# Kernel tuning notes

Hardware: AMD Instinct MI355X
Metric: run time of the kernel (lower is better)

## Reference

```python
import jax, jax.numpy as jnp
import numpy as np

D, H, S, T, NN, IN_CH, FEAT, SPA, OUT, NL, FF, E = 512, 8, 64, 32, 512, 32, 64, 32, 32, 4, 2048, 16384
NEG = 0.2  # leaky relu negative slope (GATv2 default and alpha)

def _ln(x, g, b):
    m = x.mean(-1, keepdims=True)
    v = ((x - m) ** 2).mean(-1, keepdims=True)
    return (x - m) / jnp.sqrt(v + 1e-5) * g + b

def _posenc(L):
    pos = jnp.arange(L, dtype=jnp.float32)[:, None]
    div = jnp.exp(-jnp.log(10000.0) * jnp.arange(0, D, 2, dtype=jnp.float32) / D)
    pe = jnp.zeros((L, D), jnp.float32)
    pe = pe.at[:, 0::2].set(jnp.sin(pos * div)).at[:, 1::2].set(jnp.cos(pos * div))
    return pe[:, None, :]  # (L,1,D), seq-first

def _mha(xq, xkv, wqkv, bqkv, wo, bo, mask=None):
    Lq, N, _ = xq.shape
    Lk = xkv.shape[0]
    dh = D // H
    wq, wk, wv = jnp.split(wqkv, 3, axis=1)
    bq, bk, bv = jnp.split(bqkv, 3)
    q = (xq @ wq + bq).reshape(Lq, N, H, dh)
    k = (xkv @ wk + bk).reshape(Lk, N, H, dh)
    v = (xkv @ wv + bv).reshape(Lk, N, H, dh)
    s = jnp.einsum('qnhd,knhd->nhqk', q, k) / jnp.sqrt(jnp.float32(dh))
    if mask is not None:
        s = s + mask
    a = jax.nn.softmax(s, -1)
    o = jnp.einsum('nhqk,knhd->qnhd', a, v).reshape(Lq, N, D)
    return o @ wo + bo

def _gatv2(x, wl, wr, bl, br, att, bias, e_src, e_dst):
    # GATv2: e_ij = a . leakyrelu(Wl x_j + Wr x_i); softmax over incoming edges of i; out_i = sum alpha_ij Wl x_j
    n = x.shape[0]
    h, c = att.shape
    xl = (x @ wl + bl).reshape(n, h, c)
    xr = (x @ wr + br).reshape(n, h, c)
    z = jax.nn.leaky_relu(xl[e_src] + xr[e_dst], NEG)   # (E,H,C)
    e = jnp.einsum('ehc,hc->eh', z, att)                # (E,H)
    m = jax.lax.stop_gradient(jax.ops.segment_max(e, e_dst, num_segments=n))
    ex = jnp.exp(e - m[e_dst])
    den = jax.ops.segment_sum(ex, e_dst, num_segments=n)
    alpha = ex / den[e_dst]
    out = jax.ops.segment_sum(alpha[..., None] * xl[e_src], e_dst, num_segments=n)
    return out.reshape(n, h * c) + bias

def _fwd(src, tgt, w_enc_in, b_enc_in, w_dec_in, b_dec_in, w_map, b_map,
         enc_qkv_w, enc_qkv_b, enc_out_w, enc_out_b, enc_ff1_w, enc_ff1_b, enc_ff2_w, enc_ff2_b,
         enc_ln1_g, enc_ln1_b, enc_ln2_g, enc_ln2_b, enc_fn_g, enc_fn_b,
         dec_sa_qkv_w, dec_sa_qkv_b, dec_sa_out_w, dec_sa_out_b,
         dec_ca_qkv_w, dec_ca_qkv_b, dec_ca_out_w, dec_ca_out_b,
         dec_ff1_w, dec_ff1_b, dec_ff2_w, dec_ff2_b,
         dec_ln1_g, dec_ln1_b, dec_ln2_g, dec_ln2_b, dec_ln3_g, dec_ln3_b, dec_fn_g, dec_fn_b,
         g1_wl, g1_wr, g1_bl, g1_br, g1_att, g1_bias,
         g2_wl, g2_wr, g2_bl, g2_br, g2_att, g2_bias,
         edge_index):
    # temporal transformer (eval mode, dropout off), seq-first (L, N, D)
    x = src @ w_enc_in + b_enc_in + _posenc(S)
    for i in range(NL):  # post-norm encoder, relu FFN (nn.TransformerEncoderLayer defaults)
        a = _mha(x, x, enc_qkv_w[i], enc_qkv_b[i], enc_out_w[i], enc_out_b[i])
        x = _ln(x + a, enc_ln1_g[i], enc_ln1_b[i])
        f = jax.nn.relu(x @ enc_ff1_w[i] + enc_ff1_b[i]) @ enc_ff2_w[i] + enc_ff2_b[i]
        x = _ln(x + f, enc_ln2_g[i], enc_ln2_b[i])
    mem = _ln(x, enc_fn_g, enc_fn_b)
    causal = jnp.triu(jnp.full((T, T), -1e9, jnp.float32), k=1)
    y = tgt @ w_dec_in + b_dec_in + _posenc(T)
    for i in range(NL):
        a = _mha(y, y, dec_sa_qkv_w[i], dec_sa_qkv_b[i], dec_sa_out_w[i], dec_sa_out_b[i], causal)
        y = _ln(y + a, dec_ln1_g[i], dec_ln1_b[i])
        a = _mha(y, mem, dec_ca_qkv_w[i], dec_ca_qkv_b[i], dec_ca_out_w[i], dec_ca_out_b[i])
        y = _ln(y + a, dec_ln2_g[i], dec_ln2_b[i])
        f = jax.nn.relu(y @ dec_ff1_w[i] + dec_ff1_b[i]) @ dec_ff2_w[i] + dec_ff2_b[i]
        y = _ln(y + f, dec_ln3_g[i], dec_ln3_b[i])
    y = _ln(y, dec_fn_g, dec_fn_b) @ w_map + b_map  # (T, N, FEAT)
    e_src, e_dst = edge_index[0], edge_index[1]
    def spatial(xt):  # two-layer GATv2 per time step, then elu (concat=True branch)
        h1 = _gatv2(xt, g1_wl, g1_wr, g1_bl, g1_br, g1_att, g1_bias, e_src, e_dst)
        h2 = _gatv2(h1, g2_wl, g2_wr, g2_bl, g2_br, g2_att, g2_bias, e_src, e_dst)
        return jax.nn.elu(h2)
    g = jax.vmap(spatial)(y)  # (T, N, H*OUT)
    return jax.nn.relu(g)


def setup_inputs():
    ks = iter(jax.random.split(jax.random.key(0), 100))
    def w(shape, s=0.05):
        return jax.random.normal(next(ks), shape, jnp.float32) * s
    inp = {}
    inp['src'] = jax.random.normal(next(ks), (S, NN, IN_CH), jnp.float32)
    inp['tgt'] = jax.random.normal(next(ks), (T, NN, FEAT), jnp.float32)
    inp['w_enc_in'] = w((IN_CH, D)); inp['b_enc_in'] = jnp.zeros((D,))
    inp['w_dec_in'] = w((FEAT, D)); inp['b_dec_in'] = jnp.zeros((D,))
    inp['w_map'] = w((D, FEAT)); inp['b_map'] = jnp.zeros((FEAT,))
    inp['enc_qkv_w'] = w((NL, D, 3 * D)); inp['enc_qkv_b'] = jnp.zeros((NL, 3 * D))
    inp['enc_out_w'] = w((NL, D, D)); inp['enc_out_b'] = jnp.zeros((NL, D))
    inp['enc_ff1_w'] = w((NL, D, FF)); inp['enc_ff1_b'] = jnp.zeros((NL, FF))
    inp['enc_ff2_w'] = w((NL, FF, D)); inp['enc_ff2_b'] = jnp.zeros((NL, D))
    inp['enc_ln1_g'] = jnp.ones((NL, D)); inp['enc_ln1_b'] = jnp.zeros((NL, D))
    inp['enc_ln2_g'] = jnp.ones((NL, D)); inp['enc_ln2_b'] = jnp.zeros((NL, D))
    inp['enc_fn_g'] = jnp.ones((D,)); inp['enc_fn_b'] = jnp.zeros((D,))
    inp['dec_sa_qkv_w'] = w((NL, D, 3 * D)); inp['dec_sa_qkv_b'] = jnp.zeros((NL, 3 * D))
    inp['dec_sa_out_w'] = w((NL, D, D)); inp['dec_sa_out_b'] = jnp.zeros((NL, D))
    inp['dec_ca_qkv_w'] = w((NL, D, 3 * D)); inp['dec_ca_qkv_b'] = jnp.zeros((NL, 3 * D))
    inp['dec_ca_out_w'] = w((NL, D, D)); inp['dec_ca_out_b'] = jnp.zeros((NL, D))
    inp['dec_ff1_w'] = w((NL, D, FF)); inp['dec_ff1_b'] = jnp.zeros((NL, FF))
    inp['dec_ff2_w'] = w((NL, FF, D)); inp['dec_ff2_b'] = jnp.zeros((NL, D))
    inp['dec_ln1_g'] = jnp.ones((NL, D)); inp['dec_ln1_b'] = jnp.zeros((NL, D))
    inp['dec_ln2_g'] = jnp.ones((NL, D)); inp['dec_ln2_b'] = jnp.zeros((NL, D))
    inp['dec_ln3_g'] = jnp.ones((NL, D)); inp['dec_ln3_b'] = jnp.zeros((NL, D))
    inp['dec_fn_g'] = jnp.ones((D,)); inp['dec_fn_b'] = jnp.zeros((D,))
    inp['g1_wl'] = w((FEAT, H * SPA)); inp['g1_wr'] = w((FEAT, H * SPA))
    inp['g1_bl'] = jnp.zeros((H * SPA,)); inp['g1_br'] = jnp.zeros((H * SPA,))
    inp['g1_att'] = w((H, SPA), 0.1); inp['g1_bias'] = jnp.zeros((H * SPA,))
    inp['g2_wl'] = w((H * SPA, H * OUT)); inp['g2_wr'] = w((H * SPA, H * OUT))
    inp['g2_bl'] = jnp.zeros((H * OUT,)); inp['g2_br'] = jnp.zeros((H * OUT,))
    inp['g2_att'] = w((H, OUT), 0.1); inp['g2_bias'] = jnp.zeros((H * OUT,))
    inp['edge_index'] = jax.random.randint(next(ks), (2, E), 0, NN)
    return inp


def reference(src, tgt, w_enc_in, b_enc_in, w_dec_in, b_dec_in, w_map, b_map,
              enc_qkv_w, enc_qkv_b, enc_out_w, enc_out_b, enc_ff1_w, enc_ff1_b, enc_ff2_w, enc_ff2_b,
              enc_ln1_g, enc_ln1_b, enc_ln2_g, enc_ln2_b, enc_fn_g, enc_fn_b,
              dec_sa_qkv_w, dec_sa_qkv_b, dec_sa_out_w, dec_sa_out_b,
              dec_ca_qkv_w, dec_ca_qkv_b, dec_ca_out_w, dec_ca_out_b,
              dec_ff1_w, dec_ff1_b, dec_ff2_w, dec_ff2_b,
              dec_ln1_g, dec_ln1_b, dec_ln2_g, dec_ln2_b, dec_ln3_g, dec_ln3_b, dec_fn_g, dec_fn_b,
              g1_wl, g1_wr, g1_bl, g1_br, g1_att, g1_bias,
              g2_wl, g2_wr, g2_bl, g2_br, g2_att, g2_bias,
              edge_index):
    return _fwd(src, tgt, w_enc_in, b_enc_in, w_dec_in, b_dec_in, w_map, b_map,
                enc_qkv_w, enc_qkv_b, enc_out_w, enc_out_b, enc_ff1_w, enc_ff1_b, enc_ff2_w, enc_ff2_b,
                enc_ln1_g, enc_ln1_b, enc_ln2_g, enc_ln2_b, enc_fn_g, enc_fn_b,
                dec_sa_qkv_w, dec_sa_qkv_b, dec_sa_out_w, dec_sa_out_b,
                dec_ca_qkv_w, dec_ca_qkv_b, dec_ca_out_w, dec_ca_out_b,
                dec_ff1_w, dec_ff1_b, dec_ff2_w, dec_ff2_b,
                dec_ln1_g, dec_ln1_b, dec_ln2_g, dec_ln2_b, dec_ln3_g, dec_ln3_b, dec_fn_g, dec_fn_b,
                g1_wl, g1_wr, g1_bl, g1_br, g1_att, g1_bias,
                g2_wl, g2_wr, g2_bl, g2_br, g2_att, g2_bias,
                edge_index)
```

## Files before the change

kernel.cpp:

```cpp
#include <hip/hip_runtime.h>
#include <hip/hip_bf16.h>

#define NHEAD 8
#define SLEN 64
#define TLEN 32
#define NNODE 512
#define NEDGE 16384
#define NLAYER 4

typedef __attribute__((ext_vector_type(8))) __bf16 bf16x8;
typedef __attribute__((ext_vector_type(4))) __bf16 bf16x4;
typedef __attribute__((ext_vector_type(4))) float  f32x4;

__device__ __forceinline__ void gload16(const void* g, void* l)
{
    __builtin_amdgcn_global_load_lds(
        (const __attribute__((address_space(1))) void*)g,
        (__attribute__((address_space(3))) void*)l, 16, 0, 0);
}

template<int BN>
__global__ __launch_bounds__(256) void gemm_bf16(
    const __bf16* __restrict__ A, int lda,
    const __bf16* __restrict__ Bt, int ldb,
    const float* __restrict__ bias,
    const __bf16* __restrict__ Res,
    float* __restrict__ Cf, __bf16* __restrict__ Cb, int ldc,
    int M, int N, int K, int outMode)
{
    constexpr int FM = (BN == 128) ? 4 : 2;
    __shared__ __bf16 As[128 * 64];
    __shared__ __bf16 Bs[BN * 64];
    const int tid  = threadIdx.x;
    const int wid  = tid >> 6;
    const int lane = tid & 63;
    const int wr = (BN == 128) ? (wid >> 1) : wid;
    const int wc = (BN == 128) ? (wid & 1) : 0;
    const int m0 = blockIdx.y * 128, n0 = blockIdx.x * BN;

    const int srow = wid * 8 + (lane >> 3);
    const int scol = (lane & 7) * 8;
    const int lr = lane & 15;
    const int kg = (lane >> 4) * 8;

    f32x4 acc[FM][4];
    #pragma unroll
    for (int m = 0; m < FM; ++m)
        #pragma unroll
        for (int n = 0; n < 4; ++n)
            acc[m][n] = (f32x4){0.0f, 0.0f, 0.0f, 0.0f};

    for (int k0 = 0; k0 < K; k0 += 64) {
        #pragma unroll
        for (int g = 0; g < 4; ++g) {
            const __bf16* ga = A + (size_t)(m0 + g * 32 + srow) * lda + k0 + scol;
            gload16(ga, &As[(g * 32 + wid * 8) * 64]);
        }
        #pragma unroll
        for (int g = 0; g < BN / 32; ++g) {
            const __bf16* gb = Bt + (size_t)(n0 + g * 32 + srow) * ldb + k0 + scol;
            gload16(gb, &Bs[(g * 32 + wid * 8) * 64]);
        }
        __syncthreads();
        #pragma unroll
        for (int kk = 0; kk < 64; kk += 32) {
            bf16x8 fa[FM], fb[4];
            #pragma unroll
            for (int m = 0; m < FM; ++m)
                fa[m] = *reinterpret_cast<const bf16x8*>(
                    &As[(wr * (16 * FM) + m * 16 + lr) * 64 + kk + kg]);
            #pragma unroll
            for (int n = 0; n < 4; ++n)
                fb[n] = *reinterpret_cast<const bf16x8*>(
                    &Bs[(wc * 64 + n * 16 + lr) * 64 + kk + kg]);
            #pragma unroll
            for (int m = 0; m < FM; ++m)
                #pragma unroll
                for (int n = 0; n < 4; ++n)
                    acc[m][n] = __builtin_amdgcn_mfma_f32_16x16x32_bf16(
                        fa[m], fb[n], acc[m][n], 0, 0, 0);
        }
        __syncthreads();
    }

    const int cr = (lane >> 4) * 4;
    const int cc = lane & 15;
    #pragma unroll
    for (int n = 0; n < 4; ++n) {
        const int gcol = n0 + wc * 64 + n * 16 + cc;
        const float bb = bias[gcol];
        #pragma unroll
        for (int m = 0; m < FM; ++m) {
            #pragma unroll
            for (int j = 0; j < 4; ++j) {
                const int grow = m0 + wr * (16 * FM) + m * 16 + cr + j;
                float v = acc[m][n][j] + bb;
                if (Res) v += (float)Res[(size_t)grow * ldc + gcol];
                if (outMode == 1 || outMode == 2) v = fmaxf(v, 0.0f);
                if (outMode >= 2) Cb[(size_t)grow * ldc + gcol] = (__bf16)v;
                else              Cf[(size_t)grow * ldc + gcol] = v;
            }
        }
    }
}

__global__ __launch_bounds__(256) void gemm_bias(
    const float* __restrict__ A, int lda,
    const float* __restrict__ B, int ldb,
    const float* __restrict__ bias,
    float* __restrict__ C, int ldc,
    int M, int N, int K, int relu)
{
    __shared__ float As[16][68];
    __shared__ float Bs[16][68];
    const int tid = threadIdx.x;
    const int tx = tid & 15, ty = tid >> 4;
    const int m0 = blockIdx.y * 64, n0 = blockIdx.x * 64;
    const int liA_m = tid >> 2;
    const int liA_k = (tid & 3) * 4;
    const int liB_n = (tid & 15) * 4;
    const int liB_k = tid >> 4;
    float acc[4][4] = {};
    for (int k0 = 0; k0 < K; k0 += 16) {
        float4 av = *reinterpret_cast<const float4*>(&A[(size_t)(m0 + liA_m) * lda + k0 + liA_k]);
        float4 bv = *reinterpret_cast<const float4*>(&B[(size_t)(k0 + liB_k) * ldb + n0 + liB_n]);
        As[liA_k + 0][liA_m] = av.x;
        As[liA_k + 1][liA_m] = av.y;
        As[liA_k + 2][liA_m] = av.z;
        As[liA_k + 3][liA_m] = av.w;
        *reinterpret_cast<float4*>(&Bs[liB_k][liB_n]) = bv;
        __syncthreads();
        #pragma unroll
        for (int kk = 0; kk < 16; ++kk) {
            float4 a4 = *reinterpret_cast<const float4*>(&As[kk][ty * 4]);
            float4 b4 = *reinterpret_cast<const float4*>(&Bs[kk][tx * 4]);
            float a[4] = {a4.x, a4.y, a4.z, a4.w};
            float b[4] = {b4.x, b4.y, b4.z, b4.w};
            #pragma unroll
            for (int i = 0; i < 4; ++i)
                #pragma unroll
                for (int j = 0; j < 4; ++j)
                    acc[i][j] += a[i] * b[j];
        }
        __syncthreads();
    }
    #pragma unroll
    for (int i = 0; i < 4; ++i) {
        const int m = m0 + ty * 4 + i;
        #pragma unroll
        for (int j = 0; j < 4; ++j) {
            const int n = n0 + tx * 4 + j;
            float v = acc[i][j] + bias[n];
            if (relu) v = fmaxf(v, 0.0f);
            C[(size_t)m * ldc + n] = v;
        }
    }
}

__global__ __launch_bounds__(256) void transpose_w(
    const float* __restrict__ in, __bf16* __restrict__ out, int K, int N)
{
    __shared__ __bf16 t[32][33];
    const int l = blockIdx.z;
    in  += (size_t)l * K * N;
    out += (size_t)l * K * N;
    const int k0 = blockIdx.y * 32, n0 = blockIdx.x * 32;
    const int tx = threadIdx.x & 31, ty = threadIdx.x >> 5;
    #pragma unroll
    for (int i = 0; i < 32; i += 8)
        t[ty + i][tx] = (__bf16)in[(size_t)(k0 + ty + i) * N + n0 + tx];
    __syncthreads();
    #pragma unroll
    for (int i = 0; i < 32; i += 8)
        out[(size_t)(n0 + ty + i) * K + k0 + tx] = t[tx][ty + i];
}

__global__ __launch_bounds__(256) void conv_bf16(
    const float* __restrict__ in, __bf16* __restrict__ out, int total4)
{
    const int i = blockIdx.x * 256 + threadIdx.x;
    if (i >= total4) return;
    const float4 v = *reinterpret_cast<const float4*>(&in[(size_t)i * 4]);
    bf16x4 w;
    w[0] = (__bf16)v.x; w[1] = (__bf16)v.y; w[2] = (__bf16)v.z; w[3] = (__bf16)v.w;
    *reinterpret_cast<bf16x4*>(&out[(size_t)i * 4]) = w;
}

__global__ __launch_bounds__(256) void permute_in(
    const float* __restrict__ in, float* __restrict__ out, int L, int CH, int total)
{
    const int idx = blockIdx.x * 256 + threadIdx.x;
    if (idx >= total) return;
    const int c = idx % CH;
    const int r = idx / CH;
    const int n = r & 511;
    const int l = r >> 9;
    out[((size_t)n * L + l) * CH + c] = in[idx];
}

__global__ __launch_bounds__(256) void permute_F(
    const __bf16* __restrict__ in, __bf16* __restrict__ out)
{
    const int idx = blockIdx.x * 256 + threadIdx.x;
    if (idx >= 16384 * 64) return;
    const int c = idx & 63;
    const int r = idx >> 6;
    const int n = r >> 5;
    const int t = r & 31;
    out[((size_t)(t * 512 + n)) * 64 + c] = in[idx];
}

template<int LQ, int LK, bool CAUSAL>
__global__ __launch_bounds__(64) void attn_mfma(
    const __bf16* __restrict__ Q, int ldq,
    const __bf16* __restrict__ Kp, int ldk,
    const __bf16* __restrict__ Vp, int ldv,
    __bf16* __restrict__ O, int ldo)
{
    constexpr int QF = LQ / 16, KF = LK / 16;
    constexpr int PSTR = LK + 8;
    __shared__ __bf16 Vt[64 * PSTR];
    __shared__ __bf16 Ps[LQ * PSTR];
    const int n = blockIdx.x >> 3;
    const int h = blockIdx.x & 7;
    const int lane = threadIdx.x;
    const int lr = lane & 15;
    const int g4 = lane >> 4;
    const int kg = g4 * 8;

    if (lane < LK) {
        #pragma unroll
        for (int j = 0; j < 8; ++j) {
            bf16x8 vv = *reinterpret_cast<const bf16x8*>(
                &Vp[(size_t)(n * LK + lane) * ldv + h * 64 + j * 8]);
            #pragma unroll
            for (int e = 0; e < 8; ++e)
                Vt[(j * 8 + e) * PSTR + lane] = vv[e];
        }
    }

    f32x4 s[QF][KF];
    #pragma unroll
    for (int qi = 0; qi < QF; ++qi)
        #pragma unroll
        for (int ki = 0; ki < KF; ++ki)
            s[qi][ki] = (f32x4){0.0f, 0.0f, 0.0f, 0.0f};
    #pragma unroll
    for (int kk = 0; kk < 64; kk += 32) {
        bf16x8 fa[QF], fb[KF];
        #pragma unroll
        for (int qi = 0; qi < QF; ++qi)
            fa[qi] = *reinterpret_cast<const bf16x8*>(
                &Q[(size_t)(n * LQ + qi * 16 + lr) * ldq + h * 64 + kk + kg]);
        #pragma unroll
        for (int ki = 0; ki < KF; ++ki)
            fb[ki] = *reinterpret_cast<const bf16x8*>(
                &Kp[(size_t)(n * LK + ki * 16 + lr) * ldk + h * 64 + kk + kg]);
        #pragma unroll
        for (int qi = 0; qi < QF; ++qi)
            #pragma unroll
            for (int ki = 0; ki < KF; ++ki)
                s[qi][ki] = __builtin_amdgcn_mfma_f32_16x16x32_bf16(fa[qi], fb[ki], s[qi][ki], 0, 0, 0);
    }

    float inv_s[QF][4];
    #pragma unroll
    for (int qi = 0; qi < QF; ++qi) {
        #pragma unroll
        for (int j = 0; j < 4; ++j) {
            const int row = qi * 16 + g4 * 4 + j;
            float mx = -1e30f;
            #pragma unroll
            for (int ki = 0; ki < KF; ++ki) {
                float v = s[qi][ki][j] * 0.125f;
                if (CAUSAL) { const int col = ki * 16 + lr; if (col > row) v = -1e30f; }
                s[qi][ki][j] = v;
                mx = fmaxf(mx, v);
            }
            #pragma unroll
            for (int d = 1; d < 16; d <<= 1) mx = fmaxf(mx, __shfl_xor(mx, d));
            float sum = 0.0f;
            #pragma unroll
            for (int ki = 0; ki < KF; ++ki) {
                const float p = __expf(s[qi][ki][j] - mx);
                s[qi][ki][j] = p;
                sum += p;
            }
            #pragma unroll
            for (int d = 1; d < 16; d <<= 1) sum += __shfl_xor(sum, d);
            inv_s[qi][j] = 1.0f / sum;
            #pragma unroll
            for (int ki = 0; ki < KF; ++ki)
                Ps[row * PSTR + ki * 16 + lr] = (__bf16)s[qi][ki][j];
        }
    }
    __syncthreads();

    f32x4 o[QF][4];
    #pragma unroll
    for (int qi = 0; qi < QF; ++qi)
        #pragma unroll
        for (int di = 0; di < 4; ++di)
            o[qi][di] = (f32x4){0.0f, 0.0f, 0.0f, 0.0f};
    #pragma unroll
    for (int kk = 0; kk < LK; kk += 32) {
        bf16x8 fa[QF], fb[4];
        #pragma unroll
        for (int qi = 0; qi < QF; ++qi)
            fa[qi] = *reinterpret_cast<const bf16x8*>(&Ps[(qi * 16 + lr) * PSTR + kk + kg]);
        #pragma unroll
        for (int di = 0; di < 4; ++di)
            fb[di] = *reinterpret_cast<const bf16x8*>(&Vt[(di * 16 + lr) * PSTR + kk + kg]);
        #pragma unroll
        for (int qi = 0; qi < QF; ++qi)
            #pragma unroll
            for (int di = 0; di < 4; ++di)
                o[qi][di] = __builtin_amdgcn_mfma_f32_16x16x32_bf16(fa[qi], fb[di], o[qi][di], 0, 0, 0);
    }
    #pragma unroll
    for (int qi = 0; qi < QF; ++qi)
        #pragma unroll
        for (int di = 0; di < 4; ++di)
            #pragma unroll
            for (int j = 0; j < 4; ++j) {
                const int row = qi * 16 + g4 * 4 + j;
                O[(size_t)(n * LQ + row) * ldo + h * 64 + di * 16 + lr] =
                    (__bf16)(o[qi][di][j] * inv_s[qi][j]);
            }
}

template<bool HASR, bool F32OUT>
__global__ __launch_bounds__(256) void ln_bf16(
    const __bf16* __restrict__ X, const __bf16* __restrict__ Rb,
    const float* __restrict__ g, const float* __restrict__ b,
    __bf16* __restrict__ outb, float* __restrict__ outf, int ntok)
{
    const int wid = threadIdx.x >> 6, lane = threadIdx.x & 63;
    const int row = blockIdx.x * 4 + wid;
    if (row >= ntok) return;
    const size_t base = (size_t)row * 512;
    const int c0 = lane * 8;
    const bf16x8 xv = *reinterpret_cast<const bf16x8*>(&X[base + c0]);
    float v[8];
    float s = 0.0f;
    if (HASR) {
        const bf16x8 rv = *reinterpret_cast<const bf16x8*>(&Rb[base + c0]);
        #pragma unroll
        for (int j = 0; j < 8; ++j) { v[j] = (float)xv[j] + (float)rv[j]; s += v[j]; }
    } else {
        #pragma unroll
        for (int j = 0; j < 8; ++j) { v[j] = (float)xv[j]; s += v[j]; }
    }
    #pragma unroll
    for (int d = 32; d >= 1; d >>= 1) s += __shfl_xor(s, d, 64);
    const float mean = s * (1.0f / 512.0f);
    float vs = 0.0f;
    #pragma unroll
    for (int j = 0; j < 8; ++j) { const float d = v[j] - mean; vs += d * d; }
    #pragma unroll
    for (int d = 32; d >= 1; d >>= 1) vs += __shfl_xor(vs, d, 64);
    const float rstd = rsqrtf(vs * (1.0f / 512.0f) + 1e-5f);
    const float4 g0 = *reinterpret_cast<const float4*>(&g[c0]);
    const float4 g1 = *reinterpret_cast<const float4*>(&g[c0 + 4]);
    const float4 b0 = *reinterpret_cast<const float4*>(&b[c0]);
    const float4 b1 = *reinterpret_cast<const float4*>(&b[c0 + 4]);
    const float gg[8] = {g0.x, g0.y, g0.z, g0.w, g1.x, g1.y, g1.z, g1.w};
    const float bb[8] = {b0.x, b0.y, b0.z, b0.w, b1.x, b1.y, b1.z, b1.w};
    if (F32OUT) {
        f32x4 o0, o1;
        #pragma unroll
        for (int j = 0; j < 4; ++j) o0[j] = (v[j] - mean) * rstd * gg[j] + bb[j];
        #pragma unroll
        for (int j = 0; j < 4; ++j) o1[j] = (v[4 + j] - mean) * rstd * gg[4 + j] + bb[4 + j];
        *reinterpret_cast<f32x4*>(&outf[base + c0]) = o0;
        *reinterpret_cast<f32x4*>(&outf[base + c0 + 4]) = o1;
    } else {
        bf16x8 w;
        #pragma unroll
        for (int j = 0; j < 8; ++j) w[j] = (__bf16)((v[j] - mean) * rstd * gg[j] + bb[j]);
        *reinterpret_cast<bf16x8*>(&outb[base + c0]) = w;
    }
}

__global__ __launch_bounds__(256) void add_posenc(float* __restrict__ x, int L, int total)
{
    const int idx = blockIdx.x * 256 + threadIdx.x;
    if (idx >= total) return;
    const int d = idx & 511;
    const int row = idx >> 9;
    const int l = row % L;
    const int i2 = d & ~1;
    const float freq = expf(-9.210340371976184f * (float)i2 / 512.0f);
    const float a = (float)l * freq;
    x[idx] += (d & 1) ? cosf(a) : sinf(a);
}

__global__ void zero_ints(int* __restrict__ p, int n)
{
    const int i = blockIdx.x * 256 + threadIdx.x;
    if (i < n) p[i] = 0;
}

__global__ void count_deg(const int* __restrict__ edst, int* __restrict__ deg)
{
    const int e = blockIdx.x * 256 + threadIdx.x;
    if (e < NEDGE) atomicAdd(&deg[edst[e]], 1);
}

__global__ void scan512(const int* __restrict__ deg, int* __restrict__ off)
{
    __shared__ int s[512];
    const int tid = threadIdx.x;
    s[tid] = deg[tid];
    __syncthreads();
    for (int d = 1; d < 512; d <<= 1) {
        const int t = (tid >= d) ? s[tid - d] : 0;
        __syncthreads();
        s[tid] += t;
        __syncthreads();
    }
    off[tid + 1] = s[tid];
    if (tid == 0) off[0] = 0;
}

__global__ void fill_eid(const int* __restrict__ edst, const int* __restrict__ off,
                         int* __restrict__ cur, int* __restrict__ eid)
{
    const int e = blockIdx.x * 256 + threadIdx.x;
    if (e < NEDGE) {
        const int d = edst[e];
        const int pos = off[d] + atomicAdd(&cur[d], 1);
        eid[pos] = e;
    }
}

template<bool FINAL>
__global__ __launch_bounds__(256) void gatv2_kernel(
    const float* __restrict__ xl, const float* __restrict__ xr,
    const float* __restrict__ att, const float* __restrict__ bias,
    const int* __restrict__ off, const int* __restrict__ eid,
    const int* __restrict__ esrc,
    __bf16* __restrict__ outb16, float* __restrict__ outd)
{
    const int blk = blockIdx.x;
    const int i = blk & (NNODE - 1);
    const int t = blk >> 9;
    const int tid = threadIdx.x;
    const float xrv = xr[(size_t)blk * 256 + tid];
    const float av = att[tid];
    const int e0 = off[i], e1 = off[i + 1];
    float m = -1e30f, den = 0.0f, acc = 0.0f;
    for (int idx = e0; idx < e1; ++idx) {
        const int e = eid[idx];
        const int s = esrc[e];
        const float xlv = xl[((size_t)(t * 512 + s)) * 256 + tid];
        float z = xlv + xrv;
        z = (z > 0.0f) ? z : 0.2f * z;
        float w = z * av;
        #pragma unroll
        for (int d = 16; d >= 1; d >>= 1) w += __shfl_xor(w, d, 32);
        const float mn = fmaxf(m, w);
        const float sc = __expf(m - mn);
        const float p  = __expf(w - mn);
        den = den * sc + p;
        acc = acc * sc + p * xlv;
        m = mn;
    }
    float o = (den > 0.0f) ? acc / den : 0.0f;
    o += bias[tid];
    if (FINAL) {
        o = fmaxf(o, 0.0f);
        outd[(size_t)blk * 256 + tid] = o;
    } else {
        outb16[(size_t)blk * 256 + tid] = (__bf16)o;
    }
}

extern "C" void kernel_launch(void* const* d_in, const int* in_sizes, int n_in,
                              void* d_out, int out_size, void* d_ws, size_t ws_size,
                              hipStream_t stream)
{
    const float* src       = (const float*)d_in[0];
    const float* tgt       = (const float*)d_in[1];
    const float* w_enc_in  = (const float*)d_in[2];
    const float* b_enc_in  = (const float*)d_in[3];
    const float* w_dec_in  = (const float*)d_in[4];
    const float* b_dec_in  = (const float*)d_in[5];
    const float* w_map     = (const float*)d_in[6];
    const float* b_map     = (const float*)d_in[7];
    const float* enc_qkv_w = (const float*)d_in[8];
    const float* enc_qkv_b = (const float*)d_in[9];
    const float* enc_out_w = (const float*)d_in[10];
    const float* enc_out_b = (const float*)d_in[11];
    const float* enc_ff1_w = (const float*)d_in[12];
    const float* enc_ff1_b = (const float*)d_in[13];
    const float* enc_ff2_w = (const float*)d_in[14];
    const float* enc_ff2_b = (const float*)d_in[15];
    const float* enc_ln1_g = (const float*)d_in[16];
    const float* enc_ln1_b = (const float*)d_in[17];
    const float* enc_ln2_g = (const float*)d_in[18];
    const float* enc_ln2_b = (const float*)d_in[19];
    const float* enc_fn_g  = (const float*)d_in[20];
    const float* enc_fn_b  = (const float*)d_in[21];
    const float* dec_sa_qkv_w = (const float*)d_in[22];
    const float* dec_sa_qkv_b = (const float*)d_in[23];
    const float* dec_sa_out_w = (const float*)d_in[24];
    const float* dec_sa_out_b = (const float*)d_in[25];
    const float* dec_ca_qkv_w = (const float*)d_in[26];
    const float* dec_ca_qkv_b = (const float*)d_in[27];
    const float* dec_ca_out_w = (const float*)d_in[28];
    const float* dec_ca_out_b = (const float*)d_in[29];
    const float* dec_ff1_w = (const float*)d_in[30];
    const float* dec_ff1_b = (const float*)d_in[31];
    const float* dec_ff2_w = (const float*)d_in[32];
    const float* dec_ff2_b = (const float*)d_in[33];
    const float* dec_ln1_g = (const float*)d_in[34];
    const float* dec_ln1_b = (const float*)d_in[35];
    const float* dec_ln2_g = (const float*)d_in[36];
    const float* dec_ln2_b = (const float*)d_in[37];
    const float* dec_ln3_g = (const float*)d_in[38];
    const float* dec_ln3_b = (const float*)d_in[39];
    const float* dec_fn_g  = (const float*)d_in[40];
    const float* dec_fn_b  = (const float*)d_in[41];
    const float* g1_wl   = (const float*)d_in[42];
    const float* g1_wr   = (const float*)d_in[43];
    const float* g1_bl   = (const float*)d_in[44];
    const float* g1_br   = (const float*)d_in[45];
    const float* g1_att  = (const float*)d_in[46];
    const float* g1_bias = (const float*)d_in[47];
    const float* g2_wl   = (const float*)d_in[48];
    const float* g2_wr   = (const float*)d_in[49];
    const float* g2_bl   = (const float*)d_in[50];
    const float* g2_br   = (const float*)d_in[51];
    const float* g2_att  = (const float*)d_in[52];
    const float* g2_bias = (const float*)d_in[53];
    const int*   edge_index = (const int*)d_in[54];
    const int* esrc = edge_index;
    const int* edst = edge_index + NEDGE;

    float* wsf = (float*)d_ws;
    __bf16* Xb = (__bf16*)wsf;
    __bf16* Yb = (__bf16*)(wsf + 8388608);
    float*  Rf = wsf + 12582912;
    float*  Mf = wsf + 20971520;
    float*  Wf = wsf + 29360128;
    float*  F  = wsf + 37748736;
    int* ipool = (int*)(wsf + 38797312);
    int* deg = ipool;
    int* off = deg + 512;
    int* cur = off + 516;
    int* eid = cur + 512;
    __bf16* Rb16 = (__bf16*)Rf;
    __bf16* Mb16 = (__bf16*)Mf;
    __bf16* Wb   = (__bf16*)Wf;
    __bf16* midb = (__bf16*)Rf;

    auto gemm = [&](const float* A, int lda, const float* B, int ldb, const float* bias,
                    float* Cc, int ldc, int M, int N, int K, int relu) {
        dim3 grid((unsigned)(N / 64), (unsigned)(M / 64));
        gemm_bias<<<grid, 256, 0, stream>>>(A, lda, B, ldb, bias, Cc, ldc, M, N, K, relu);
    };
    auto gemmT = [&](const __bf16* A, int lda, const __bf16* Bt, int ldb,
                     const float* bias, const __bf16* Res, float* Cf, __bf16* Cb, int ldc,
                     int M, int N, int K, int mode) {
        dim3 grid((unsigned)(N / 128), (unsigned)(M / 128));
        gemm_bf16<128><<<grid, 256, 0, stream>>>(A, lda, Bt, ldb, bias, Res, Cf, Cb, ldc, M, N, K, mode);
    };
    auto gemmT64 = [&](const __bf16* A, int lda, const __bf16* Bt, int ldb,
                       const float* bias, const __bf16* Res, float* Cf, __bf16* Cb, int ldc,
                       int M, int N, int K, int mode) {
        dim3 grid((unsigned)(N / 64), (unsigned)(M / 128));
        gemm_bf16<64><<<grid, 256, 0, stream>>>(A, lda, Bt, ldb, bias, Res, Cf, Cb, ldc, M, N, K, mode);
    };
    auto tw = [&](const float* w, __bf16* o, int K, int N, int L) {
        dim3 g((unsigned)(N / 32), (unsigned)(K / 32), (unsigned)L);
        transpose_w<<<g, 256, 0, stream>>>(w, o, K, N);
    };

    zero_ints<<<8, 256, 0, stream>>>(ipool, 512 + 516 + 512);
    count_deg<<<NEDGE / 256, 256, 0, stream>>>(edst, deg);
    scan512<<<1, 512, 0, stream>>>(deg, off);
    fill_eid<<<NEDGE / 256, 256, 0, stream>>>(edst, off, cur, eid);

    {
        float* src_nm = Wf;
        float* Xtmp = Rf;
        permute_in<<<4096, 256, 0, stream>>>(src, src_nm, SLEN, 32, 32768 * 32);
        gemm(src_nm, 32, w_enc_in, 512, b_enc_in, Xtmp, 512, 32768, 512, 32, 0);
        add_posenc<<<(32768 * 512) / 256, 256, 0, stream>>>(Xtmp, SLEN, 32768 * 512);
        conv_bf16<<<16384, 256, 0, stream>>>(Xtmp, Xb, 32768 * 128);
        float* tgt_nm = Wf;
        float* Ytmp = Rf;
        permute_in<<<4096, 256, 0, stream>>>(tgt, tgt_nm, TLEN, 64, 16384 * 64);
        gemm(tgt_nm, 64, w_dec_in, 512, b_dec_in, Ytmp, 512, 16384, 512, 64, 0);
        add_posenc<<<(16384 * 512) / 256, 256, 0, stream>>>(Ytmp, TLEN, 16384 * 512);
        conv_bf16<<<8192, 256, 0, stream>>>(Ytmp, Yb, 16384 * 128);
    }

    __bf16* WeQkv = Wb + 0;
    __bf16* WeOut = Wb + 3145728;
    __bf16* WeFf1 = Wb + 4194304;
    __bf16* WeFf2 = Wb + 8388608;
    tw(enc_qkv_w, WeQkv, 512, 1536, NLAYER);
    tw(enc_out_w, WeOut, 512, 512, NLAYER);
    tw(enc_ff1_w, WeFf1, 512, 2048, NLAYER);
    tw(enc_ff2_w, WeFf2, 2048, 512, NLAYER);

    for (int i = 0; i < NLAYER; ++i) {
        for (int c = 0; c < 4; ++c) {
            gemmT(Xb + (size_t)c * 8192 * 512, 512, WeQkv + (size_t)i * 786432, 512,
                  enc_qkv_b + (size_t)i * 1536, nullptr, nullptr, Rb16, 1536, 8192, 1536, 512, 3);
            attn_mfma<64, 64, false><<<1024, 64, 0, stream>>>(
                Rb16, 1536, Rb16 + 512, 1536, Rb16 + 1024, 1536,
                Mb16 + (size_t)c * 8192 * 512, 512);
        }
        gemmT(Mb16, 512, WeOut + (size_t)i * 262144, 512, enc_out_b + (size_t)i * 512,
              Xb, nullptr, Xb, 512, 32768, 512, 512, 3);
        ln_bf16<false, false><<<8192, 256, 0, stream>>>(Xb, nullptr,
            enc_ln1_g + (size_t)i * 512, enc_ln1_b + (size_t)i * 512, Xb, nullptr, 32768);
        for (int s = 0; s < 2; ++s) {
            gemmT(Xb + (size_t)s * 16384 * 512, 512, WeFf1 + (size_t)i * 1048576, 512,
                  enc_ff1_b + (size_t)i * 2048, nullptr, nullptr, midb, 2048, 16384, 2048, 512, 2);
            gemmT64(midb, 2048, WeFf2 + (size_t)i * 1048576, 2048,
                    enc_ff2_b + (size_t)i * 512, Xb + (size_t)s * 16384 * 512,
                    nullptr, Xb + (size_t)s * 16384 * 512, 512, 16384, 512, 2048, 3);
        }
        ln_bf16<false, false><<<8192, 256, 0, stream>>>(Xb, nullptr,
            enc_ln2_g + (size_t)i * 512, enc_ln2_b + (size_t)i * 512, Xb, nullptr, 32768);
    }
    ln_bf16<false, false><<<8192, 256, 0, stream>>>(Xb, nullptr, enc_fn_g, enc_fn_b,
                                                    Xb, nullptr, 32768);

    __bf16* WdSaQkv = Wb + 0;
    __bf16* WdSaOut = Wb + 3145728;
    __bf16* WdCaQkv = Wb + 4194304;
    __bf16* WdCaOut = Wb + 7340032;
    __bf16* WdFf1   = Wb + 8388608;
    __bf16* WdFf2   = Wb + 12582912;
    tw(dec_sa_qkv_w, WdSaQkv, 512, 1536, NLAYER);
    tw(dec_sa_out_w, WdSaOut, 512, 512, NLAYER);
    tw(dec_ca_qkv_w, WdCaQkv, 512, 1536, NLAYER);
    tw(dec_ca_out_w, WdCaOut, 512, 512, NLAYER);
    tw(dec_ff1_w,    WdFf1,   512, 2048, NLAYER);
    tw(dec_ff2_w,    WdFf2,   2048, 512, NLAYER);

    __bf16* ObD  = Mb16;
    __bf16* QbC  = Mb16;
    __bf16* ObCA = (__bf16*)(Mf + 4194304);
    for (int i = 0; i < NLAYER; ++i) {
        for (int c = 0; c < 2; ++c) {
            gemmT(Yb + (size_t)c * 8192 * 512, 512, WdSaQkv + (size_t)i * 786432, 512,
                  dec_sa_qkv_b + (size_t)i * 1536, nullptr, nullptr, Rb16, 1536, 8192, 1536, 512, 3);
            attn_mfma<32, 32, true><<<2048, 64, 0, stream>>>(
                Rb16, 1536, Rb16 + 512, 1536, Rb16 + 1024, 1536,
                ObD + (size_t)c * 8192 * 512, 512);
        }
        gemmT64(ObD, 512, WdSaOut + (size_t)i * 262144, 512, dec_sa_out_b + (size_t)i * 512,
                Yb, nullptr, Yb, 512, 16384, 512, 512, 3);
        ln_bf16<false, false><<<4096, 256, 0, stream>>>(Yb, nullptr,
            dec_ln1_g + (size_t)i * 512, dec_ln1_b + (size_t)i * 512, Yb, nullptr, 16384);
        gemmT64(Yb, 512, WdCaQkv + (size_t)i * 786432, 512,
                dec_ca_qkv_b + (size_t)i * 1536, nullptr, nullptr, QbC, 512, 16384, 512, 512, 3);
        for (int c = 0; c < 2; ++c) {
            gemmT(Xb + (size_t)c * 16384 * 512, 512, WdCaQkv + (size_t)i * 786432 + 262144, 512,
                  dec_ca_qkv_b + (size_t)i * 1536 + 512, nullptr, nullptr, Rb16, 1024, 16384, 1024, 512, 3);
            attn_mfma<32, 64, false><<<2048, 64, 0, stream>>>(
                QbC + (size_t)c * 8192 * 512, 512, Rb16, 1024, Rb16 + 512, 1024,
                ObCA + (size_t)c * 8192 * 512, 512);
        }
        gemmT64(ObCA, 512, WdCaOut + (size_t)i * 262144, 512, dec_ca_out_b + (size_t)i * 512,
                Yb, nullptr, Yb, 512, 16384, 512, 512, 3);
        ln_bf16<false, false><<<4096, 256, 0, stream>>>(Yb, nullptr,
            dec_ln2_g + (size_t)i * 512, dec_ln2_b + (size_t)i * 512, Yb, nullptr, 16384);
        gemmT(Yb, 512, WdFf1 + (size_t)i * 1048576, 512,
              dec_ff1_b + (size_t)i * 2048, nullptr, nullptr, midb, 2048, 16384, 2048, 512, 2);
        gemmT64(midb, 2048, WdFf2 + (size_t)i * 1048576, 2048,
                dec_ff2_b + (size_t)i * 512, Yb, nullptr, Yb, 512, 16384, 512, 2048, 3);
        ln_bf16<false, false><<<4096, 256, 0, stream>>>(Yb, nullptr,
            dec_ln3_g + (size_t)i * 512, dec_ln3_b + (size_t)i * 512, Yb, nullptr, 16384);
    }
    ln_bf16<false, false><<<4096, 256, 0, stream>>>(Yb, nullptr, dec_fn_g, dec_fn_b,
                                                    Yb, nullptr, 16384);

    __bf16* Wmapt = Wb;
    __bf16* G1wlT = Wb + 32768;
    __bf16* G1wrT = Wb + 49152;
    __bf16* G2wlT = Wb + 65536;
    __bf16* G2wrT = Wb + 131072;
    __bf16* Ftb   = Wb + 196608;
    __bf16* Ibb   = Wb + 1245184;
    tw(w_map, Wmapt, 512, 64, 1);
    tw(g1_wl, G1wlT, 64, 256, 1);
    tw(g1_wr, G1wrT, 64, 256, 1);
    tw(g2_wl, G2wlT, 256, 256, 1);
    tw(g2_wr, G2wrT, 256, 256, 1);

    __bf16* Fb16 = (__bf16*)F;
    gemmT64(Yb, 512, Wmapt, 512, b_map, nullptr, nullptr, Fb16, 64, 16384, 64, 512, 3);
    permute_F<<<4096, 256, 0, stream>>>(Fb16, Ftb);

    float* G  = Mf;
    float* Hb = Mf + 4194304;
    gemmT64(Ftb, 64, G1wlT, 64, g1_bl, nullptr, G,  nullptr, 256, 16384, 256, 64, 0);
    gemmT64(Ftb, 64, G1wrT, 64, g1_br, nullptr, Hb, nullptr, 256, 16384, 256, 64, 0);
    gatv2_kernel<false><<<16384, 256, 0, stream>>>(G, Hb, g1_att, g1_bias, off, eid, esrc,
                                                   Ibb, nullptr);
    gemmT64(Ibb, 256, G2wlT, 256, g2_bl, nullptr, G,  nullptr, 256, 16384, 256, 256, 0);
    gemmT64(Ibb, 256, G2wrT, 256, g2_br, nullptr, Hb, nullptr, 256, 16384, 256, 256, 0);
    gatv2_kernel<true><<<16384, 256, 0, stream>>>(G, Hb, g2_att, g2_bias, off, eid, esrc,
                                                  nullptr, (float*)d_out);
}
```

Baseline: 4.839 ms.

## Move residual add into layernorm, shrink FFN chunks, and batch GATv2 edge loop

```diff
diff --git a/kernel.cpp b/kernel.cpp
--- a/kernel.cpp
+++ b/kernel.cpp
@@ -450,21 +450,35 @@
     const float av = att[tid];
     const int e0 = off[i], e1 = off[i + 1];
     float m = -1e30f, den = 0.0f, acc = 0.0f;
-    for (int idx = e0; idx < e1; ++idx) {
-        const int e = eid[idx];
-        const int s = esrc[e];
-        const float xlv = xl[((size_t)(t * 512 + s)) * 256 + tid];
-        float z = xlv + xrv;
-        z = (z > 0.0f) ? z : 0.2f * z;
-        float w = z * av;
-        #pragma unroll
-        for (int d = 16; d >= 1; d >>= 1) w += __shfl_xor(w, d, 32);
-        const float mn = fmaxf(m, w);
+    for (int base = e0; base < e1; base += 16) {
+        float xv[16], ws[16];
+        float tm = -1e30f;
+        #pragma unroll
+        for (int k = 0; k < 16; ++k) {
+            const int idx = base + k;
+            float w = -1e30f, xlv = 0.0f;
+            if (idx < e1) {
+                const int s = esrc[eid[idx]];
+                xlv = xl[((size_t)(t * 512 + s)) * 256 + tid];
+                float z = xlv + xrv;
+                z = (z > 0.0f) ? z : 0.2f * z;
+                w = z * av;
+                #pragma unroll
+                for (int d = 16; d >= 1; d >>= 1) w += __shfl_xor(w, d, 32);
+            }
+            ws[k] = w;
+            xv[k] = xlv;
+            tm = fmaxf(tm, w);
+        }
+        const float mn = fmaxf(m, tm);
         const float sc = __expf(m - mn);
-        const float p  = __expf(w - mn);
-        den = den * sc + p;
-        acc = acc * sc + p * xlv;
-        m = mn;
+        den *= sc; acc *= sc; m = mn;
+        #pragma unroll
+        for (int k = 0; k < 16; ++k) {
+            const float p = __expf(ws[k] - m);
+            den += p;
+            acc += p * xv[k];
+        }
     }
     float o = (den > 0.0f) ? acc / den : 0.0f;
     o += bias[tid];
@@ -553,7 +567,6 @@
     __bf16* Rb16 = (__bf16*)Rf;
     __bf16* Mb16 = (__bf16*)Mf;
     __bf16* Wb   = (__bf16*)Wf;
-    __bf16* midb = (__bf16*)Rf;
 
     auto gemm = [&](const float* A, int lda, const float* B, int ldb, const float* bias,
                     float* Cc, int ldc, int M, int N, int K, int relu) {
@@ -561,16 +574,16 @@
         gemm_bias<<<grid, 256, 0, stream>>>(A, lda, B, ldb, bias, Cc, ldc, M, N, K, relu);
     };
     auto gemmT = [&](const __bf16* A, int lda, const __bf16* Bt, int ldb,
-                     const float* bias, const __bf16* Res, float* Cf, __bf16* Cb, int ldc,
+                     const float* bias, float* Cf, __bf16* Cb, int ldc,
                      int M, int N, int K, int mode) {
         dim3 grid((unsigned)(N / 128), (unsigned)(M / 128));
-        gemm_bf16<128><<<grid, 256, 0, stream>>>(A, lda, Bt, ldb, bias, Res, Cf, Cb, ldc, M, N, K, mode);
+        gemm_bf16<128><<<grid, 256, 0, stream>>>(A, lda, Bt, ldb, bias, nullptr, Cf, Cb, ldc, M, N, K, mode);
     };
     auto gemmT64 = [&](const __bf16* A, int lda, const __bf16* Bt, int ldb,
-                       const float* bias, const __bf16* Res, float* Cf, __bf16* Cb, int ldc,
+                       const float* bias, float* Cf, __bf16* Cb, int ldc,
                        int M, int N, int K, int mode) {
         dim3 grid((unsigned)(N / 64), (unsigned)(M / 128));
-        gemm_bf16<64><<<grid, 256, 0, stream>>>(A, lda, Bt, ldb, bias, Res, Cf, Cb, ldc, M, N, K, mode);
+        gemm_bf16<64><<<grid, 256, 0, stream>>>(A, lda, Bt, ldb, bias, nullptr, Cf, Cb, ldc, M, N, K, mode);
     };
     auto tw = [&](const float* w, __bf16* o, int K, int N, int L) {
         dim3 g((unsigned)(N / 32), (unsigned)(K / 32), (unsigned)L);
@@ -609,23 +622,23 @@
     for (int i = 0; i < NLAYER; ++i) {
         for (int c = 0; c < 4; ++c) {
             gemmT(Xb + (size_t)c * 8192 * 512, 512, WeQkv + (size_t)i * 786432, 512,
-                  enc_qkv_b + (size_t)i * 1536, nullptr, nullptr, Rb16, 1536, 8192, 1536, 512, 3);
+                  enc_qkv_b + (size_t)i * 1536, nullptr, Rb16, 1536, 8192, 1536, 512, 3);
             attn_mfma<64, 64, false><<<1024, 64, 0, stream>>>(
                 Rb16, 1536, Rb16 + 512, 1536, Rb16 + 1024, 1536,
                 Mb16 + (size_t)c * 8192 * 512, 512);
         }
         gemmT(Mb16, 512, WeOut + (size_t)i * 262144, 512, enc_out_b + (size_t)i * 512,
-              Xb, nullptr, Xb, 512, 32768, 512, 512, 3);
-        ln_bf16<false, false><<<8192, 256, 0, stream>>>(Xb, nullptr,
+              nullptr, Rb16, 512, 32768, 512, 512, 3);
+        ln_bf16<true, false><<<8192, 256, 0, stream>>>(Xb, Rb16,
             enc_ln1_g + (size_t)i * 512, enc_ln1_b + (size_t)i * 512, Xb, nullptr, 32768);
-        for (int s = 0; s < 2; ++s) {
-            gemmT(Xb + (size_t)s * 16384 * 512, 512, WeFf1 + (size_t)i * 1048576, 512,
-                  enc_ff1_b + (size_t)i * 2048, nullptr, nullptr, midb, 2048, 16384, 2048, 512, 2);
-            gemmT64(midb, 2048, WeFf2 + (size_t)i * 1048576, 2048,
-                    enc_ff2_b + (size_t)i * 512, Xb + (size_t)s * 16384 * 512,
-                    nullptr, Xb + (size_t)s * 16384 * 512, 512, 16384, 512, 2048, 3);
-        }
-        ln_bf16<false, false><<<8192, 256, 0, stream>>>(Xb, nullptr,
+        for (int s = 0; s < 4; ++s) {
+            gemmT(Xb + (size_t)s * 8192 * 512, 512, WeFf1 + (size_t)i * 1048576, 512,
+                  enc_ff1_b + (size_t)i * 2048, nullptr, Mb16, 2048, 8192, 2048, 512, 2);
+            gemmT64(Mb16, 2048, WeFf2 + (size_t)i * 1048576, 2048,
+                    enc_ff2_b + (size_t)i * 512, nullptr, Rb16 + (size_t)s * 8192 * 512, 512,
+                    8192, 512, 2048, 3);
+        }
+        ln_bf16<true, false><<<8192, 256, 0, stream>>>(Xb, Rb16,
             enc_ln2_g + (size_t)i * 512, enc_ln2_b + (size_t)i * 512, Xb, nullptr, 32768);
     }
     ln_bf16<false, false><<<8192, 256, 0, stream>>>(Xb, nullptr, enc_fn_g, enc_fn_b,
@@ -646,37 +659,40 @@
 
     __bf16* ObD  = Mb16;
     __bf16* QbC  = Mb16;
-    __bf16* ObCA = (__bf16*)(Mf + 4194304);
+    __bf16* ObCA = (__bf16*)(Mf + 2097152);
     for (int i = 0; i < NLAYER; ++i) {
         for (int c = 0; c < 2; ++c) {
             gemmT(Yb + (size_t)c * 8192 * 512, 512, WdSaQkv + (size_t)i * 786432, 512,
-                  dec_sa_qkv_b + (size_t)i * 1536, nullptr, nullptr, Rb16, 1536, 8192, 1536, 512, 3);
+                  dec_sa_qkv_b + (size_t)i * 1536, nullptr, Rb16, 1536, 8192, 1536, 512, 3);
             attn_mfma<32, 32, true><<<2048, 64, 0, stream>>>(
                 Rb16, 1536, Rb16 + 512, 1536, Rb16 + 1024, 1536,
                 ObD + (size_t)c * 8192 * 512, 512);
         }
         gemmT64(ObD, 512, WdSaOut + (size_t)i * 262144, 512, dec_sa_out_b + (size_t)i * 512,
-                Yb, nullptr, Yb, 512, 16384, 512, 512, 3);
-        ln_bf16<false, false><<<4096, 256, 0, stream>>>(Yb, nullptr,
+                nullptr, Rb16, 512, 16384, 512, 512, 3);
+        ln_bf16<true, false><<<4096, 256, 0, stream>>>(Yb, Rb16,
             dec_ln1_g + (size_t)i * 512, dec_ln1_b + (size_t)i * 512, Yb, nullptr, 16384);
-        gemmT64(Yb, 512, WdCaQkv + (size_t)i * 786432, 512,
-                dec_ca_qkv_b + (size_t)i * 1536, nullptr, nullptr, QbC, 512, 16384, 512, 512, 3);
         for (int c = 0; c < 2; ++c) {
+            gemmT64(Yb + (size_t)c * 8192 * 512, 512, WdCaQkv + (size_t)i * 786432, 512,
+                    dec_ca_qkv_b + (size_t)i * 1536, nullptr, QbC, 512, 8192, 512, 512, 3);
             gemmT(Xb + (size_t)c * 16384 * 512, 512, WdCaQkv + (size_t)i * 786432 + 262144, 512,
-                  dec_ca_qkv_b + (size_t)i * 1536 + 512, nullptr, nullptr, Rb16, 1024, 16384, 1024, 512, 3);
+                  dec_ca_qkv_b + (size_t)i * 1536 + 512, nullptr, Rb16, 1024, 16384, 1024, 512, 3);
             attn_mfma<32, 64, false><<<2048, 64, 0, stream>>>(
-                QbC + (size_t)c * 8192 * 512, 512, Rb16, 1024, Rb16 + 512, 1024,
+                QbC, 512, Rb16, 1024, Rb16 + 512, 1024,
                 ObCA + (size_t)c * 8192 * 512, 512);
         }
         gemmT64(ObCA, 512, WdCaOut + (size_t)i * 262144, 512, dec_ca_out_b + (size_t)i * 512,
-                Yb, nullptr, Yb, 512, 16384, 512, 512, 3);
-        ln_bf16<false, false><<<4096, 256, 0, stream>>>(Yb, nullptr,
+                nullptr, Rb16, 512, 16384, 512, 512, 3);
+        ln_bf16<true, false><<<4096, 256, 0, stream>>>(Yb, Rb16,
             dec_ln2_g + (size_t)i * 512, dec_ln2_b + (size_t)i * 512, Yb, nullptr, 16384);
-        gemmT(Yb, 512, WdFf1 + (size_t)i * 1048576, 512,
-              dec_ff1_b + (size_t)i * 2048, nullptr, nullptr, midb, 2048, 16384, 2048, 512, 2);
-        gemmT64(midb, 2048, WdFf2 + (size_t)i * 1048576, 2048,
-                dec_ff2_b + (size_t)i * 512, Yb, nullptr, Yb, 512, 16384, 512, 2048, 3);
-        ln_bf16<false, false><<<4096, 256, 0, stream>>>(Yb, nullptr,
+        for (int s = 0; s < 2; ++s) {
+            gemmT(Yb + (size_t)s * 8192 * 512, 512, WdFf1 + (size_t)i * 1048576, 512,
+                  dec_ff1_b + (size_t)i * 2048, nullptr, Mb16, 2048, 8192, 2048, 512, 2);
+            gemmT64(Mb16, 2048, WdFf2 + (size_t)i * 1048576, 2048,
+                    dec_ff2_b + (size_t)i * 512, nullptr, Rb16 + (size_t)s * 8192 * 512, 512,
+                    8192, 512, 2048, 3);
+        }
+        ln_bf16<true, false><<<4096, 256, 0, stream>>>(Yb, Rb16,
             dec_ln3_g + (size_t)i * 512, dec_ln3_b + (size_t)i * 512, Yb, nullptr, 16384);
     }
     ln_bf16<false, false><<<4096, 256, 0, stream>>>(Yb, nullptr, dec_fn_g, dec_fn_b,
@@ -696,17 +712,17 @@
     tw(g2_wr, G2wrT, 256, 256, 1);
 
     __bf16* Fb16 = (__bf16*)F;
-    gemmT64(Yb, 512, Wmapt, 512, b_map, nullptr, nullptr, Fb16, 64, 16384, 64, 512, 3);
+    gemmT64(Yb, 512, Wmapt, 512, b_map, nullptr, Fb16, 64, 16384, 64, 512, 3);
     permute_F<<<4096, 256, 0, stream>>>(Fb16, Ftb);
 
     float* G  = Mf;
     float* Hb = Mf + 4194304;
-    gemmT64(Ftb, 64, G1wlT, 64, g1_bl, nullptr, G,  nullptr, 256, 16384, 256, 64, 0);
-    gemmT64(Ftb, 64, G1wrT, 64, g1_br, nullptr, Hb, nullptr, 256, 16384, 256, 64, 0);
+    gemmT64(Ftb, 64, G1wlT, 64, g1_bl, G,  nullptr, 256, 16384, 256, 64, 0);
+    gemmT64(Ftb, 64, G1wrT, 64, g1_br, Hb, nullptr, 256, 16384, 256, 64, 0);
     gatv2_kernel<false><<<16384, 256, 0, stream>>>(G, Hb, g1_att, g1_bias, off, eid, esrc,
                                                    Ibb, nullptr);
-    gemmT64(Ibb, 256, G2wlT, 256, g2_bl, nullptr, G,  nullptr, 256, 16384, 256, 256, 0);
-    gemmT64(Ibb, 256, G2wrT, 256, g2_br, nullptr, Hb, nullptr, 256, 16384, 256, 256, 0);
+    gemmT64(Ibb, 256, G2wlT, 256, g2_bl, G,  nullptr, 256, 16384, 256, 256, 0);
+    gemmT64(Ibb, 256, G2wrT, 256, g2_br, Hb, nullptr, 256, 16384, 256, 256, 0);
     gatv2_kernel<true><<<16384, 256, 0, stream>>>(G, Hb, g2_att, g2_bias, off, eid, esrc,
                                                   nullptr, (float*)d_out);
 }
```

Measured after the change: 4.766 ms. About the same (-1.5%).
